# Kernel optimization log

Hardware: AMD Instinct MI355X
Metric: run time of the kernel (lower is better)

The kernel has to match this reference:

```python
import jax, jax.numpy as jnp
import numpy as np

T, N, E, D, H = 128, 1024, 16384, 256, 8


def setup_inputs() -> dict:
    key = jax.random.key(0)
    ks = jax.random.split(key, 8)
    s = 0.02  # weight init scale
    return {
        "embeddings": jax.random.normal(ks[0], (T, N, D), jnp.float32),
        "W1": jax.random.normal(ks[1], (D, 2 * D), jnp.float32) * s,
        "b1": jnp.zeros((2 * D,), jnp.float32),
        "W2": jax.random.normal(ks[2], (2 * D, D), jnp.float32) * s,
        "b2": jnp.zeros((D,), jnp.float32),
        "Wq": jax.random.normal(ks[3], (D, D), jnp.float32) * s,
        "bq": jnp.zeros((D,), jnp.float32),
        "Wk": jax.random.normal(ks[4], (D, D), jnp.float32) * s,
        "bk": jnp.zeros((D,), jnp.float32),
        "edge_val": jax.random.uniform(ks[5], (T, E), jnp.float32),
        "edge_src": jax.random.randint(ks[6], (T, E), 0, N),
        "edge_dst": jax.random.randint(ks[7], (T, E), 0, N),
    }


def _pos_encoding(t, d):
    # sin/cos interleaved positional encoding, pe[:,0::2]=sin, pe[:,1::2]=cos
    pos = jnp.arange(t, dtype=jnp.float32)[:, None]
    div = jnp.exp(jnp.arange(0, d, 2, dtype=jnp.float32) * (-np.log(10000.0) / d))
    ang = pos * div  # [t, d//2]
    return jnp.stack([jnp.sin(ang), jnp.cos(ang)], axis=-1).reshape(t, d)


def reference(embeddings, W1, b1, W2, b2, Wq, bq, Wk, bk, edge_val, edge_src, edge_dst):
    t, n, d = embeddings.shape
    hd = d // H
    # per-timestep node MLP + avg/max pooling over nodes  -> one vector per snapshot
    h = jax.nn.relu(embeddings @ W1 + b1)          # [T, N, 2D]
    pooled = h.mean(axis=1) + h.max(axis=1)        # [T, 2D] (adaptive avg+max pool to 1)
    x = jax.nn.relu(pooled @ W2 + b2)              # [T, D]
    x = x + _pos_encoding(t, d)
    # multi-head self-attention probabilities (batch=1), averaged over heads
    q = ((x @ Wq + bq) * (hd ** -0.5)).reshape(t, H, hd)
    k = (x @ Wk + bk).reshape(t, H, hd)
    scores = jnp.einsum('qhd,khd->hqk', q, k)      # [H, T, T]
    probs = jax.nn.softmax(scores, axis=-1).mean(axis=0)  # [T, T]
    # threshold, add identity, causal (lower-triangular) mask
    probs = jnp.where(probs < 1.0 / t, 0.0, probs)
    probs = (probs + jnp.eye(t, dtype=probs.dtype)) * jnp.tril(jnp.ones((t, t), probs.dtype))
    # build adjacency stack from edge lists (COO scatter), then weighted accumulation
    t_idx = jnp.arange(t)[:, None]
    A = jnp.zeros((t, n, n), embeddings.dtype).at[t_idx, edge_src, edge_dst].add(edge_val)
    # new_At[t] = sum_s probs[t, s] * A[s]
    return jnp.einsum('ts,snm->tnm', probs, A)
```

## Files before the change

kernel.cpp:

```cpp
#include <hip/hip_runtime.h>
#include <hip/hip_bf16.h>

#define T_ 128
#define N_ 1024
#define E_ 16384
#define D_ 256
#define H_ 8
#define D2_ 512
#define NB2_ 4096
#define PS3_ 257

typedef __attribute__((ext_vector_type(8))) short bf16x8;
typedef __attribute__((ext_vector_type(4))) float f32x4;

__device__ __forceinline__ void atomAddF(float* p, float v) {
#if defined(__HIP_PLATFORM_AMD__)
    unsafeAtomicAdd(p, v);
#else
    atomicAdd(p, v);
#endif
}

__device__ __forceinline__ unsigned short f2bf(float x) {
    return __bfloat16_as_ushort(__float2bfloat16(x));
}

__global__ __launch_bounds__(256)
void k_prep(const float* __restrict__ W1, unsigned short* __restrict__ W1S,
            const int* __restrict__ edge_src, const int* __restrict__ edge_dst,
            float4* __restrict__ poolz, int* __restrict__ cnt)
{
    __shared__ int hist[NB2_];
    const int bi = blockIdx.x, tid = threadIdx.x;
    const int s = bi >> 1, h = bi & 1;

    if (tid < 128) poolz[bi * 128 + tid] = make_float4(0.f, 0.f, 0.f, 0.f);

    if (tid < 64) {
        const int u   = bi * 64 + tid;
        const int col = u & 511;
        const int k8  = u >> 9;
        unsigned short hh[8];
        #pragma unroll
        for (int j = 0; j < 8; ++j)
            hh[j] = f2bf(W1[(size_t)(k8 * 8 + j) * D2_ + col]);
        uint4 pk;
        pk.x = hh[0] | ((unsigned)hh[1] << 16);
        pk.y = hh[2] | ((unsigned)hh[3] << 16);
        pk.z = hh[4] | ((unsigned)hh[5] << 16);
        pk.w = hh[6] | ((unsigned)hh[7] << 16);
        *(uint4*)&W1S[(size_t)k8 * 4096 + col * 8] = pk;
    }

    for (int i = tid; i < NB2_; i += 256) hist[i] = 0;
    __syncthreads();
    const int e0 = h * 8192;
    for (int e = e0 + tid; e < e0 + 8192; e += 256) {
        const size_t eo = (size_t)s * E_ + e;
        atomicAdd(&hist[(edge_src[eo] << 2) | (edge_dst[eo] >> 8)], 1);
    }
    __syncthreads();
    const int slot = (s << 1) | h;
    for (int i = tid; i < NB2_; i += 256) cnt[i * 256 + slot] = hist[i];
}

__global__ __launch_bounds__(512)
void k_mlp1_mfma(const float* __restrict__ emb,
                 const unsigned short* __restrict__ W1S,
                 const float* __restrict__ b1,
                 float* __restrict__ pool_sum,
                 unsigned int* __restrict__ pool_max)
{
    __shared__ unsigned short A_l[2048];
    __shared__ unsigned short B_l[16384];

    const int tid  = threadIdx.x;
    const int lane = tid & 63;
    const int wave = tid >> 6;
    const int wm = wave >> 2, wn = wave & 3;
    const int l15 = lane & 15, l4 = lane >> 4;
    const int r0 = blockIdx.x * 64;
    const int t  = blockIdx.x >> 4;

    f32x4 acc[2][8] = {};

    for (int ks = 0; ks < 8; ++ks) {
        {
            const int row = tid >> 3, k4 = tid & 7;
            const float4 v = *(const float4*)&emb[(size_t)(r0 + row) * D_ + ks * 32 + k4 * 4];
            uint2 pk;
            pk.x = f2bf(v.x) | ((unsigned)f2bf(v.y) << 16);
            pk.y = f2bf(v.z) | ((unsigned)f2bf(v.w) << 16);
            *(uint2*)&A_l[(k4 >> 1) * 512 + row * 8 + (k4 & 1) * 4] = pk;
        }
        {
            const char* gsrc = (const char*)W1S + (size_t)ks * 32768;
            #pragma unroll
            for (int r = 0; r < 4; ++r) {
                const int off = r * 8192 + tid * 16;
                __builtin_amdgcn_global_load_lds(
                    (const __attribute__((address_space(1))) unsigned int*)(gsrc + off),
                    (__attribute__((address_space(3))) unsigned int*)((char*)B_l + off),
                    16, 0, 0);
            }
        }
        __syncthreads();

        const bf16x8 a0 = *(const bf16x8*)&A_l[l4 * 512 + (wm * 32 + l15) * 8];
        const bf16x8 a1 = *(const bf16x8*)&A_l[l4 * 512 + (wm * 32 + 16 + l15) * 8];
        #pragma unroll
        for (int cf = 0; cf < 8; ++cf) {
            const bf16x8 b = *(const bf16x8*)&B_l[l4 * 4096 + (wn * 128 + cf * 16 + l15) * 8];
            acc[0][cf] = __builtin_amdgcn_mfma_f32_16x16x32_bf16(a0, b, acc[0][cf], 0, 0, 0);
            acc[1][cf] = __builtin_amdgcn_mfma_f32_16x16x32_bf16(a1, b, acc[1][cf], 0, 0, 0);
        }
        __syncthreads();
    }

    #pragma unroll
    for (int cf = 0; cf < 8; ++cf) {
        const int col = wn * 128 + cf * 16 + l15;
        const float bias = b1[col];
        float cs = 0.f, cm = 0.f;
        #pragma unroll
        for (int mf = 0; mf < 2; ++mf) {
            #pragma unroll
            for (int j = 0; j < 4; ++j) {
                float hh = acc[mf][cf][j] + bias;
                hh = fmaxf(hh, 0.f);
                cs += hh;
                cm = fmaxf(cm, hh);
            }
        }
        cs += __shfl_xor(cs, 16);
        cs += __shfl_xor(cs, 32);
        cm = fmaxf(cm, __shfl_xor(cm, 16));
        cm = fmaxf(cm, __shfl_xor(cm, 32));
        if (l4 == 0) {
            atomAddF(pool_sum + t * D2_ + col, cs);
            atomicMax(pool_max + t * D2_ + col, __float_as_uint(cm));
        }
    }
}

__global__ __launch_bounds__(256)
void k_scan3(const int* __restrict__ cnt, unsigned short* __restrict__ prefS3,
             int* __restrict__ totB)
{
    __shared__ int sc[256];
    const int b = blockIdx.x, tid = threadIdx.x;
    sc[tid] = cnt[b * 256 + tid];
    __syncthreads();
    #pragma unroll
    for (int off = 1; off < 256; off <<= 1) {
        int v = (tid >= off) ? sc[tid - off] : 0;
        __syncthreads();
        sc[tid] += v;
        __syncthreads();
    }
    prefS3[b * PS3_ + tid + 1] = (unsigned short)sc[tid];
    if (tid == 0)   prefS3[b * PS3_] = 0;
    if (tid == 255) totB[b] = sc[255];
}

__global__ __launch_bounds__(256)
void k_scatter3(const float* __restrict__ edge_val,
                const int* __restrict__ edge_src,
                const int* __restrict__ edge_dst,
                const unsigned short* __restrict__ prefS3,
                const int* __restrict__ totB,
                int* __restrict__ segB,
                uint2* __restrict__ sortedC)
{
    __shared__ int bst[NB2_];
    const int bi = blockIdx.x, tid = threadIdx.x;
    const int s = bi >> 1, h = bi & 1;
    const int slot = (s << 1) | h;

    int orig[16];
    #pragma unroll
    for (int r = 0; r < 16; ++r) {
        const int i = r * 256 + tid;
        orig[r] = totB[i];
        bst[i] = orig[r];
    }
    __syncthreads();
    for (int off = 1; off < NB2_; off <<= 1) {
        int tmp[16];
        #pragma unroll
        for (int r = 0; r < 16; ++r) {
            const int i = r * 256 + tid;
            tmp[r] = (i >= off) ? bst[i - off] : 0;
        }
        __syncthreads();
        #pragma unroll
        for (int r = 0; r < 16; ++r) bst[r * 256 + tid] += tmp[r];
        __syncthreads();
    }
    #pragma unroll
    for (int r = 0; r < 16; ++r) {
        const int i = r * 256 + tid;
        const int excl = bst[i] - orig[r];
        if (bi == 0) {
            #pragma unroll
            for (int kcx = 0; kcx < 5; ++kcx)
                segB[i * 5 + kcx] = excl + (int)prefS3[i * PS3_ + kcx * 64];
        }
        bst[i] = excl + (int)prefS3[i * PS3_ + slot];
    }
    __syncthreads();

    const int e0 = h * 8192;
    for (int e = e0 + tid; e < e0 + 8192; e += 256) {
        const size_t eo = (size_t)s * E_ + e;
        const int src = edge_src[eo];
        const int dst = edge_dst[eo];
        const float v = edge_val[eo];
        const int bkt = (src << 2) | (dst >> 8);
        const int gidx = atomicAdd(&bst[bkt], 1);
        sortedC[gidx] = make_uint2((unsigned)((s << 8) | (dst & 255)),
                                   __float_as_uint(v));
    }
}

__global__ __launch_bounds__(256)
void k_mlp2qk(const float* __restrict__ pool_sum,
              const unsigned int* __restrict__ pool_max,
              const float* __restrict__ W2, const float* __restrict__ b2,
              const float* __restrict__ Wq, const float* __restrict__ bq,
              const float* __restrict__ Wk, const float* __restrict__ bk,
              float* __restrict__ q, float* __restrict__ k)
{
    __shared__ float pl[D2_];
    __shared__ float xl[D_];
    const int t = blockIdx.x;
    const int j = threadIdx.x;

    pl[j]       = pool_sum[t * D2_ + j]       * (1.0f / (float)N_) +
                  __uint_as_float(pool_max[t * D2_ + j]);
    pl[j + 256] = pool_sum[t * D2_ + j + 256] * (1.0f / (float)N_) +
                  __uint_as_float(pool_max[t * D2_ + j + 256]);
    __syncthreads();

    float acc = b2[j];
    for (int kk = 0; kk < D2_; ++kk)
        acc += pl[kk] * W2[(size_t)kk * D_ + j];
    acc = fmaxf(acc, 0.f);

    const int i2 = (j >> 1) * 2;
    const float div = expf((float)i2 * (-logf(10000.0f) / (float)D_));
    const float ang = (float)t * div;
    acc += (j & 1) ? cosf(ang) : sinf(ang);
    xl[j] = acc;
    __syncthreads();

    float aq = bq[j], ak = bk[j];
    for (int kk = 0; kk < D_; ++kk) {
        const float xv = xl[kk];
        aq += xv * Wq[(size_t)kk * D_ + j];
        ak += xv * Wk[(size_t)kk * D_ + j];
    }
    q[t * D_ + j] = aq * 0.17677669529663687f;
    k[t * D_ + j] = ak;
}

__global__ __launch_bounds__(128)
void k_probs(const float* __restrict__ q,
             const float* __restrict__ k,
             float* __restrict__ probs)
{
    __shared__ float ql[D_];
    __shared__ float red[128];
    const int qt = blockIdx.x;
    const int kt = threadIdx.x;

    ql[kt]       = q[qt * D_ + kt];
    ql[kt + 128] = q[qt * D_ + kt + 128];
    __syncthreads();

    float sh[H_];
    #pragma unroll
    for (int h = 0; h < H_; ++h) {
        float s = 0.f;
        #pragma unroll
        for (int d = 0; d < 32; ++d)
            s += ql[h * 32 + d] * k[kt * D_ + h * 32 + d];
        sh[h] = s;
    }

    float pm = 0.f;
    for (int h = 0; h < H_; ++h) {
        red[kt] = sh[h]; __syncthreads();
        for (int off = 64; off > 0; off >>= 1) {
            if (kt < off) red[kt] = fmaxf(red[kt], red[kt + off]);
            __syncthreads();
        }
        const float m = red[0]; __syncthreads();
        const float e = expf(sh[h] - m);
        red[kt] = e; __syncthreads();
        for (int off = 64; off > 0; off >>= 1) {
            if (kt < off) red[kt] += red[kt + off];
            __syncthreads();
        }
        const float Z = red[0]; __syncthreads();
        pm += e / Z;
    }
    pm *= (1.0f / (float)H_);

    if (pm < (1.0f / (float)T_)) pm = 0.f;
    if (kt == qt) pm += 1.0f;
    if (kt > qt) pm = 0.f;
    probs[qt * T_ + kt] = pm;
}

__global__ __launch_bounds__(256)
void k_pcast(const float* __restrict__ probs, unsigned short* __restrict__ Pfrag)
{
    const int u    = blockIdx.x * 256 + threadIdx.x;
    const int lane = u & 63;
    const int tf   = (u >> 6) & 7;
    const int kc   = u >> 9;
    const int t    = tf * 16 + (lane & 15);
    const int s0   = kc * 32 + (lane >> 4) * 8;
    unsigned short hh[8];
    #pragma unroll
    for (int j = 0; j < 8; ++j)
        hh[j] = f2bf(probs[t * T_ + s0 + j]);
    uint4 pk;
    pk.x = hh[0] | ((unsigned)hh[1] << 16);
    pk.y = hh[2] | ((unsigned)hh[3] << 16);
    pk.z = hh[4] | ((unsigned)hh[5] << 16);
    pk.w = hh[6] | ((unsigned)hh[7] << 16);
    *(uint4*)&Pfrag[u * 8] = pk;
}

__global__ __launch_bounds__(256)
void k_accum_mfma(const unsigned short* __restrict__ Pfrag,
                  const uint2* __restrict__ sortedC,
                  const int* __restrict__ segB,
                  float* __restrict__ out)
{
    __shared__ float stage[32 * 258];
    __shared__ unsigned short P_l[16384];

    const int ct   = blockIdx.x;
    const int tid  = threadIdx.x;
    const int lane = tid & 63;
    const int wv   = tid >> 6;
    const int l15  = lane & 15, l4 = lane >> 4;

    #pragma unroll
    for (int r = 0; r < 8; ++r) {
        const int off = r * 4096 + tid * 16;
        __builtin_amdgcn_global_load_lds(
            (const __attribute__((address_space(1))) unsigned int*)((const char*)Pfrag + off),
            (__attribute__((address_space(3))) unsigned int*)((char*)P_l + off),
            16, 0, 0);
    }

    const int sb = ct * 5;
    f32x4 acc[8][4] = {};

    for (int kc = 0; kc < 4; ++kc) {
        __syncthreads();
        {
            float4* s4 = (float4*)stage;
            for (int i = tid; i < 2064; i += 256)
                s4[i] = make_float4(0.f, 0.f, 0.f, 0.f);
        }
        __syncthreads();
        const int i0 = segB[sb + kc];
        const int i1 = segB[sb + kc + 1];
        for (int i = i0 + tid; i < i1; i += 256) {
            const uint2 it = sortedC[i];
            atomicAdd(&stage[((it.x >> 8) & 31) * 258 + (it.x & 255)],
                      __uint_as_float(it.y));
        }
        __syncthreads();

        #pragma unroll
        for (int cf = 0; cf < 4; ++cf) {
            const int c = wv * 64 + cf * 16 + l15;
            float bs[8];
            #pragma unroll
            for (int j = 0; j < 8; ++j)
                bs[j] = stage[(l4 * 8 + j) * 258 + c];
            bf16x8 bfr;
            #pragma unroll
            for (int j = 0; j < 8; ++j)
                bfr[j] = (short)f2bf(bs[j]);
            #pragma unroll
            for (int tf = 0; tf < 8; ++tf) {
                if (tf >= 2 * kc) {
                    const bf16x8 af =
                        *(const bf16x8*)&P_l[((kc * 8 + tf) * 64 + lane) * 8];
                    acc[tf][cf] = __builtin_amdgcn_mfma_f32_16x16x32_bf16(
                        af, bfr, acc[tf][cf], 0, 0, 0);
                }
            }
        }
    }

    const int erow = tid >> 6;
    const int ecol = (tid & 63) * 4;
    #pragma unroll
    for (int tf = 0; tf < 8; ++tf) {
        __syncthreads();
        #pragma unroll
        for (int cf = 0; cf < 4; ++cf) {
            const int c = wv * 64 + cf * 16 + l15;
            #pragma unroll
            for (int j = 0; j < 4; ++j)
                stage[(l4 * 4 + j) * 260 + c] = acc[tf][cf][j];
        }
        __syncthreads();
        #pragma unroll
        for (int ii = 0; ii < 4; ++ii) {
            const int row = ii * 4 + erow;
            const float4 v = *(const float4*)&stage[row * 260 + ecol];
            *(float4*)&out[((size_t)(tf * 16 + row) << 20) + ct * 256 + ecol] = v;
        }
    }
}

extern "C" void kernel_launch(void* const* d_in, const int* in_sizes, int n_in,
                              void* d_out, int out_size, void* d_ws, size_t ws_size,
                              hipStream_t stream) {
    const float* emb      = (const float*)d_in[0];
    const float* W1       = (const float*)d_in[1];
    const float* b1       = (const float*)d_in[2];
    const float* W2       = (const float*)d_in[3];
    const float* b2       = (const float*)d_in[4];
    const float* Wq       = (const float*)d_in[5];
    const float* bq       = (const float*)d_in[6];
    const float* Wk       = (const float*)d_in[7];
    const float* bk       = (const float*)d_in[8];
    const float* edge_val = (const float*)d_in[9];
    const int*   edge_src = (const int*)d_in[10];
    const int*   edge_dst = (const int*)d_in[11];
    float* out = (float*)d_out;

    char* ws = (char*)d_ws;
    float*          pool_sum = (float*)(ws);
    unsigned int*   pool_max = (unsigned int*)(ws + (256 << 10));
    float*          q        = (float*)(ws + (512 << 10));
    float*          k        = (float*)(ws + (640 << 10));
    float*          probs    = (float*)(ws + (768 << 10));
    unsigned short* W1S      = (unsigned short*)(ws + (832 << 10));
    unsigned short* Pfrag    = (unsigned short*)(ws + (1088 << 10));
    int*            totB     = (int*)(ws + (1120 << 10));
    int*            segB     = (int*)(ws + (1136 << 10));
    unsigned short* prefS3   = (unsigned short*)(ws + (1216 << 10));
    int*            cnt      = (int*)(ws + (3328 << 10));
    uint2*          sortedC  = (uint2*)(ws + (3328 << 10));

    k_prep<<<256, 256, 0, stream>>>(W1, W1S, edge_src, edge_dst,
                                    (float4*)pool_sum, cnt);
    k_mlp1_mfma<<<2048, 512, 0, stream>>>(emb, W1S, b1, pool_sum, pool_max);
    k_scan3<<<NB2_, 256, 0, stream>>>(cnt, prefS3, totB);
    k_scatter3<<<256, 256, 0, stream>>>(edge_val, edge_src, edge_dst,
                                        prefS3, totB, segB, sortedC);
    k_mlp2qk<<<128, 256, 0, stream>>>(pool_sum, pool_max, W2, b2,
                                      Wq, bq, Wk, bk, q, k);
    k_probs<<<128, 128, 0, stream>>>(q, k, probs);
    k_pcast<<<8, 256, 0, stream>>>(probs, Pfrag);
    k_accum_mfma<<<NB2_, 256, 0, stream>>>(Pfrag, sortedC, segB, out);
}
```

Before: 358.5 us.

## Fuse bf16 cast into probs kernel, streamline scans, nontemporal output stores

Four separate changes. The scatter kernel's 4096-entry block scan becomes a per-thread serial sum of 16 values followed by a 256-wide block scan, which cuts the number of barriers. The softmax reductions in k_probs now use wavefront shuffles instead of shared-memory tree reductions. k_probs also writes the bf16 MFMA fragments directly, which removes the k_pcast launch and the float probs buffer. The accumulate epilogue stages two t-fragments per barrier pair with a padded stride and writes the 512MB output with nontemporal stores to avoid cache pollution.

```diff
diff --git a/kernel.cpp b/kernel.cpp
--- a/kernel.cpp
+++ b/kernel.cpp
@@ -172,35 +172,37 @@
                 int* __restrict__ segB,
                 uint2* __restrict__ sortedC)
 {
+    __shared__ int sc[256];
     __shared__ int bst[NB2_];
     const int bi = blockIdx.x, tid = threadIdx.x;
     const int s = bi >> 1, h = bi & 1;
     const int slot = (s << 1) | h;
 
-    int orig[16];
+    int v[16];
+    int run = 0;
+    const int4* t4 = (const int4*)&totB[tid * 16];
+    #pragma unroll
+    for (int r4 = 0; r4 < 4; ++r4) {
+        const int4 x = t4[r4];
+        v[r4 * 4 + 0] = x.x; v[r4 * 4 + 1] = x.y;
+        v[r4 * 4 + 2] = x.z; v[r4 * 4 + 3] = x.w;
+        run += x.x + x.y + x.z + x.w;
+    }
+    sc[tid] = run;
+    __syncthreads();
+    #pragma unroll
+    for (int off = 1; off < 256; off <<= 1) {
+        int u = (tid >= off) ? sc[tid - off] : 0;
+        __syncthreads();
+        sc[tid] += u;
+        __syncthreads();
+    }
+    int p = sc[tid] - run;
     #pragma unroll
     for (int r = 0; r < 16; ++r) {
-        const int i = r * 256 + tid;
-        orig[r] = totB[i];
-        bst[i] = orig[r];
-    }
-    __syncthreads();
-    for (int off = 1; off < NB2_; off <<= 1) {
-        int tmp[16];
-        #pragma unroll
-        for (int r = 0; r < 16; ++r) {
-            const int i = r * 256 + tid;
-            tmp[r] = (i >= off) ? bst[i - off] : 0;
-        }
-        __syncthreads();
-        #pragma unroll
-        for (int r = 0; r < 16; ++r) bst[r * 256 + tid] += tmp[r];
-        __syncthreads();
-    }
-    #pragma unroll
-    for (int r = 0; r < 16; ++r) {
-        const int i = r * 256 + tid;
-        const int excl = bst[i] - orig[r];
+        const int i = tid * 16 + r;
+        const int excl = p;
+        p += v[r];
         if (bi == 0) {
             #pragma unroll
             for (int kcx = 0; kcx < 5; ++kcx)
@@ -215,11 +217,11 @@
         const size_t eo = (size_t)s * E_ + e;
         const int src = edge_src[eo];
         const int dst = edge_dst[eo];
-        const float v = edge_val[eo];
+        const float vv = edge_val[eo];
         const int bkt = (src << 2) | (dst >> 8);
         const int gidx = atomicAdd(&bst[bkt], 1);
         sortedC[gidx] = make_uint2((unsigned)((s << 8) | (dst & 255)),
-                                   __float_as_uint(v));
+                                   __float_as_uint(vv));
     }
 }
 
@@ -267,12 +269,15 @@
 __global__ __launch_bounds__(128)
 void k_probs(const float* __restrict__ q,
              const float* __restrict__ k,
-             float* __restrict__ probs)
+             unsigned short* __restrict__ Pfrag)
 {
     __shared__ float ql[D_];
-    __shared__ float red[128];
+    __shared__ float wmax[2][H_];
+    __shared__ float wsum[2][H_];
+    __shared__ float pall[T_];
     const int qt = blockIdx.x;
     const int kt = threadIdx.x;
+    const int wv = kt >> 6, ln = kt & 63;
 
     ql[kt]       = q[qt * D_ + kt];
     ql[kt + 128] = q[qt * D_ + kt + 128];
@@ -288,50 +293,55 @@
         sh[h] = s;
     }
 
+    #pragma unroll
+    for (int h = 0; h < H_; ++h) {
+        float v = sh[h];
+        #pragma unroll
+        for (int off = 32; off > 0; off >>= 1)
+            v = fmaxf(v, __shfl_xor(v, off));
+        if (ln == 0) wmax[wv][h] = v;
+    }
+    __syncthreads();
+    float e[H_];
+    #pragma unroll
+    for (int h = 0; h < H_; ++h) {
+        const float m = fmaxf(wmax[0][h], wmax[1][h]);
+        e[h] = expf(sh[h] - m);
+        float v = e[h];
+        #pragma unroll
+        for (int off = 32; off > 0; off >>= 1)
+            v += __shfl_xor(v, off);
+        if (ln == 0) wsum[wv][h] = v;
+    }
+    __syncthreads();
     float pm = 0.f;
-    for (int h = 0; h < H_; ++h) {
-        red[kt] = sh[h]; __syncthreads();
-        for (int off = 64; off > 0; off >>= 1) {
-            if (kt < off) red[kt] = fmaxf(red[kt], red[kt + off]);
-            __syncthreads();
-        }
-        const float m = red[0]; __syncthreads();
-        const float e = expf(sh[h] - m);
-        red[kt] = e; __syncthreads();
-        for (int off = 64; off > 0; off >>= 1) {
-            if (kt < off) red[kt] += red[kt + off];
-            __syncthreads();
-        }
-        const float Z = red[0]; __syncthreads();
-        pm += e / Z;
-    }
+    #pragma unroll
+    for (int h = 0; h < H_; ++h)
+        pm += e[h] / (wsum[0][h] + wsum[1][h]);
     pm *= (1.0f / (float)H_);
 
     if (pm < (1.0f / (float)T_)) pm = 0.f;
     if (kt == qt) pm += 1.0f;
     if (kt > qt) pm = 0.f;
-    probs[qt * T_ + kt] = pm;
-}
-
-__global__ __launch_bounds__(256)
-void k_pcast(const float* __restrict__ probs, unsigned short* __restrict__ Pfrag)
-{
-    const int u    = blockIdx.x * 256 + threadIdx.x;
-    const int lane = u & 63;
-    const int tf   = (u >> 6) & 7;
-    const int kc   = u >> 9;
-    const int t    = tf * 16 + (lane & 15);
-    const int s0   = kc * 32 + (lane >> 4) * 8;
-    unsigned short hh[8];
-    #pragma unroll
-    for (int j = 0; j < 8; ++j)
-        hh[j] = f2bf(probs[t * T_ + s0 + j]);
-    uint4 pk;
-    pk.x = hh[0] | ((unsigned)hh[1] << 16);
-    pk.y = hh[2] | ((unsigned)hh[3] << 16);
-    pk.z = hh[4] | ((unsigned)hh[5] << 16);
-    pk.w = hh[6] | ((unsigned)hh[7] << 16);
-    *(uint4*)&Pfrag[u * 8] = pk;
+    pall[kt] = pm;
+    __syncthreads();
+
+    if (kt < 16) {
+        const int kc = kt >> 2, g = kt & 3;
+        const int lane = g * 16 + (qt & 15);
+        const int u = kc * 512 + (qt >> 4) * 64 + lane;
+        const int s0 = kc * 32 + g * 8;
+        unsigned short hh[8];
+        #pragma unroll
+        for (int j = 0; j < 8; ++j)
+            hh[j] = f2bf(pall[s0 + j]);
+        uint4 pk;
+        pk.x = hh[0] | ((unsigned)hh[1] << 16);
+        pk.y = hh[2] | ((unsigned)hh[3] << 16);
+        pk.z = hh[4] | ((unsigned)hh[5] << 16);
+        pk.w = hh[6] | ((unsigned)hh[7] << 16);
+        *(uint4*)&Pfrag[u * 8] = pk;
+    }
 }
 
 __global__ __launch_bounds__(256)
@@ -340,7 +350,7 @@
                   const int* __restrict__ segB,
                   float* __restrict__ out)
 {
-    __shared__ float stage[32 * 258];
+    __shared__ float stage[8576];
     __shared__ unsigned short P_l[16384];
 
     const int ct   = blockIdx.x;
@@ -404,21 +414,30 @@
     const int erow = tid >> 6;
     const int ecol = (tid & 63) * 4;
     #pragma unroll
-    for (int tf = 0; tf < 8; ++tf) {
-        __syncthreads();
-        #pragma unroll
-        for (int cf = 0; cf < 4; ++cf) {
-            const int c = wv * 64 + cf * 16 + l15;
-            #pragma unroll
-            for (int j = 0; j < 4; ++j)
-                stage[(l4 * 4 + j) * 260 + c] = acc[tf][cf][j];
-        }
-        __syncthreads();
-        #pragma unroll
-        for (int ii = 0; ii < 4; ++ii) {
-            const int row = ii * 4 + erow;
-            const float4 v = *(const float4*)&stage[row * 260 + ecol];
-            *(float4*)&out[((size_t)(tf * 16 + row) << 20) + ct * 256 + ecol] = v;
+    for (int tp = 0; tp < 4; ++tp) {
+        __syncthreads();
+        #pragma unroll
+        for (int sl = 0; sl < 2; ++sl) {
+            const int tf = tp * 2 + sl;
+            #pragma unroll
+            for (int cf = 0; cf < 4; ++cf) {
+                const int c = wv * 64 + cf * 16 + l15;
+                #pragma unroll
+                for (int j = 0; j < 4; ++j)
+                    stage[sl * 4288 + (l4 * 4 + j) * 268 + c] = acc[tf][cf][j];
+            }
+        }
+        __syncthreads();
+        #pragma unroll
+        for (int sl = 0; sl < 2; ++sl) {
+            const int tf = tp * 2 + sl;
+            #pragma unroll
+            for (int ii = 0; ii < 4; ++ii) {
+                const int row = ii * 4 + erow;
+                const f32x4 vv = *(const f32x4*)&stage[sl * 4288 + row * 268 + ecol];
+                __builtin_nontemporal_store(vv,
+                    (f32x4*)&out[((size_t)(tf * 16 + row) << 20) + ct * 256 + ecol]);
+            }
         }
     }
 }
@@ -445,7 +464,6 @@
     unsigned int*   pool_max = (unsigned int*)(ws + (256 << 10));
     float*          q        = (float*)(ws + (512 << 10));
     float*          k        = (float*)(ws + (640 << 10));
-    float*          probs    = (float*)(ws + (768 << 10));
     unsigned short* W1S      = (unsigned short*)(ws + (832 << 10));
     unsigned short* Pfrag    = (unsigned short*)(ws + (1088 << 10));
     int*            totB     = (int*)(ws + (1120 << 10));
@@ -462,7 +480,6 @@
                                         prefS3, totB, segB, sortedC);
     k_mlp2qk<<<128, 256, 0, stream>>>(pool_sum, pool_max, W2, b2,
                                       Wq, bq, Wk, bk, q, k);
-    k_probs<<<128, 128, 0, stream>>>(q, k, probs);
-    k_pcast<<<8, 256, 0, stream>>>(probs, Pfrag);
+    k_probs<<<128, 128, 0, stream>>>(q, k, Pfrag);
     k_accum_mfma<<<NB2_, 256, 0, stream>>>(Pfrag, sortedC, segB, out);
 }
```

Result: faster. 292.5 us, median of 2 (-18.4%).
